# Kernel optimization log

Measured on AMD Instinct MI355X. Metric: run time of the kernel, lower is better.

Reference implementation:

```python
import jax, jax.numpy as jnp
import numpy as np
from itertools import product

NEIGH = (3, 3, 3)  # attn_neighbourhood_size


def setup_inputs() -> dict:
    key = jax.random.key(0)
    b, h, d = 2, 8, 16
    H = W = D = 24
    x = jax.random.normal(key, (b, h, H * W * D, d), dtype=jnp.float32)
    return {"x": x, "height": H, "width": W, "depth": D}


def _localize_3d(x, height, width, depth):
    # x: [b, h, n, d] with n = height*width*depth
    b, hh, n, d = x.shape
    kh, kw, kd = NEIGH
    ph, pw, pd = kh // 2, kw // 2, kd // 2  # 'same' padding for odd kernels
    vol = x.reshape(b, hh, height, width, depth, d)
    padded = jnp.pad(vol, ((0, 0), (0, 0), (ph, ph), (pw, pw), (pd, pd), (0, 0)))
    # conv3d with a unit impulse at (i,j,k) (cross-correlation) is exactly the
    # shifted slice padded[..., i:i+H, j:j+W, k:k+D, :]; filter order is i,j,k.
    shifts = [
        padded[:, :, i:i + height, j:j + width, k:k + depth, :]
        for i, j, k in product(range(kh), range(kw), range(kd))
    ]
    out = jnp.stack(shifts, axis=-2)  # [b, h, H, W, D, filter_n, d]
    return out.reshape(b, hh, n, kh * kw * kd, d)


def reference(x, height, width, depth):
    return _localize_3d(x, height, width, depth)
```

## Files before the change

kernel.cpp:

```cpp
#include <hip/hip_runtime.h>


#define GH 24
#define GW 24
#define GD 24
#define NPOS (GH * GW * GD)
#define NBH 16
#define NDIM 16
#define NF 27


__global__ __launch_bounds__(256) void localize3d_kernel(
    const float4* __restrict__ in,
    float4* __restrict__ out,
    unsigned int total4)
{
    unsigned int stride = gridDim.x * blockDim.x;
    for (unsigned int o = blockIdx.x * blockDim.x + threadIdx.x; o < total4; o += stride) {
        unsigned int dd4 = o & 3u;
        unsigned int r   = o >> 2;
        unsigned int f   = r % NF;
        unsigned int r2  = r / NF;
        unsigned int pos = r2 % NPOS;
        unsigned int bh  = r2 / NPOS;

        unsigned int z  = pos % GD;
        unsigned int xy = pos / GD;
        unsigned int x  = xy % GW;
        unsigned int y  = xy / GW;

        unsigned int fi = f / 9u;
        unsigned int fj = (f / 3u) % 3u;
        unsigned int fk = f % 3u;

        int ny = (int)y + (int)fi - 1;
        int nx = (int)x + (int)fj - 1;
        int nz = (int)z + (int)fk - 1;

        float4 v = make_float4(0.f, 0.f, 0.f, 0.f);
        if ((unsigned)ny < GH && (unsigned)nx < GW && (unsigned)nz < GD) {
            unsigned int npos = ((unsigned)ny * GW + (unsigned)nx) * GD + (unsigned)nz;
            v = in[(bh * NPOS + npos) * 4u + dd4];
        }
        out[o] = v;
    }
}

extern "C" void kernel_launch(void* const* d_in, const int* in_sizes, int n_in,
                              void* d_out, int out_size, void* d_ws, size_t ws_size,
                              hipStream_t stream) {
    const float4* in = (const float4*)d_in[0];
    float4* out = (float4*)d_out;

    unsigned int total4 = (unsigned int)(out_size / 4);
    const int block = 256;
    unsigned int nblocks = (total4 + block - 1) / block;
    if (nblocks > 2048u) nblocks = 2048u;

    localize3d_kernel<<<nblocks, block, 0, stream>>>(in, out, total4);
}
```

Baseline: 425.5 us.

## Stage input neighbourhood slab in LDS and write outputs from shared memory

Each block now owns one (bh, y, 4-wide x tile) output slab and first loads the padded 3x6x26 input neighbourhood into LDS, with zero fill at the borders. It then streams the 27 shifted copies to global memory from LDS using incremental index arithmetic instead of per-element divisions. This targets repeated global/L2 reads of the same inputs and costly integer div/mod. The grid is hard-coded to the fixed 24^3 shape and 16 batch-heads, so the kernel is no longer generic.

```diff
diff --git a/kernel.cpp b/kernel.cpp
--- a/kernel.cpp
+++ b/kernel.cpp
@@ -1,61 +1,76 @@
 #include <hip/hip_runtime.h>
 
 
-#define GH 24
-#define GW 24
-#define GD 24
-#define NPOS (GH * GW * GD)
-#define NBH 16
-#define NDIM 16
 #define NF 27
 
+typedef float4 f4;
 
-__global__ __launch_bounds__(256) void localize3d_kernel(
-    const float4* __restrict__ in,
-    float4* __restrict__ out,
-    unsigned int total4)
+__global__ __launch_bounds__(256) void localize3d_lds(
+    const f4* __restrict__ in,
+    f4* __restrict__ out)
 {
-    unsigned int stride = gridDim.x * blockDim.x;
-    for (unsigned int o = blockIdx.x * blockDim.x + threadIdx.x; o < total4; o += stride) {
-        unsigned int dd4 = o & 3u;
-        unsigned int r   = o >> 2;
-        unsigned int f   = r % NF;
-        unsigned int r2  = r / NF;
-        unsigned int pos = r2 % NPOS;
-        unsigned int bh  = r2 / NPOS;
+    __shared__ f4 slab[1872];
 
-        unsigned int z  = pos % GD;
-        unsigned int xy = pos / GD;
-        unsigned int x  = xy % GW;
-        unsigned int y  = xy / GW;
+    unsigned bid = blockIdx.x;
+    unsigned xt = bid % 6u;
+    unsigned y  = (bid / 6u) % 24u;
+    unsigned bh = bid / 144u;
+    unsigned x0 = xt * 4u;
 
-        unsigned int fi = f / 9u;
-        unsigned int fj = (f / 3u) % 3u;
-        unsigned int fk = f % 3u;
+    for (unsigned s = threadIdx.x; s < 1872u; s += 256u) {
+        unsigned dd4 = s & 3u;
+        unsigned sv  = s >> 2;
+        unsigned sz  = sv % 26u;
+        unsigned sx  = (sv / 26u) % 6u;
+        unsigned sy  = sv / 156u;
+        int gy = (int)y  + (int)sy - 1;
+        int gx = (int)x0 + (int)sx - 1;
+        int gz = (int)sz - 1;
+        f4 v = make_float4(0.f, 0.f, 0.f, 0.f);
+        if ((unsigned)gy < 24u && (unsigned)gx < 24u && (unsigned)gz < 24u) {
+            unsigned q = ((bh * 24u + (unsigned)gy) * 24u + (unsigned)gx) * 24u + (unsigned)gz;
+            v = in[q * 4u + dd4];
+        }
+        slab[s] = v;
+    }
+    __syncthreads();
 
-        int ny = (int)y + (int)fi - 1;
-        int nx = (int)x + (int)fj - 1;
-        int nz = (int)z + (int)fk - 1;
+    unsigned t   = threadIdx.x;
+    unsigned dd4 = t & 3u;
+    unsigned r0  = t >> 2;
+    unsigned lv  = r0 / 27u;
+    unsigned f   = r0 - lv * 27u;
+    unsigned lx  = 0u;
+    unsigned lz  = lv;
 
-        float4 v = make_float4(0.f, 0.f, 0.f, 0.f);
-        if ((unsigned)ny < GH && (unsigned)nx < GW && (unsigned)nz < GD) {
-            unsigned int npos = ((unsigned)ny * GW + (unsigned)nx) * GD + (unsigned)nz;
-            v = in[(bh * NPOS + npos) * 4u + dd4];
-        }
-        out[o] = v;
-    }
+    unsigned q0 = ((bh * 24u + y) * 24u + x0) * 24u;
+    unsigned ob = q0 * 108u + t;
+
+#define BODY() do {                                                     \
+        unsigned fi = (f * 57u) >> 9;                \
+        unsigned f3 = (f * 171u) >> 9;               \
+        unsigned fj = f3 - fi * 3u;                                     \
+        unsigned fk = f - f3 * 3u;                                      \
+        unsigned sv = (fi * 6u + lx + fj) * 26u + (lz + fk);            \
+        out[ob] = slab[sv * 4u + dd4];                                  \
+        ob += 256u;                                                     \
+        f += 10u;                             \
+        unsigned inc = 2u;                                              \
+        if (f >= 27u) { f -= 27u; inc = 3u; }                           \
+        lz += inc;                                                      \
+        if (lz >= 24u) { lz -= 24u; lx += 1u; }                         \
+    } while (0)
+
+#pragma unroll 4
+    for (int k = 0; k < 40; ++k) { BODY(); }
+    if (t < 128u) { BODY(); }
+#undef BODY
 }
 
 extern "C" void kernel_launch(void* const* d_in, const int* in_sizes, int n_in,
                               void* d_out, int out_size, void* d_ws, size_t ws_size,
                               hipStream_t stream) {
-    const float4* in = (const float4*)d_in[0];
-    float4* out = (float4*)d_out;
-
-    unsigned int total4 = (unsigned int)(out_size / 4);
-    const int block = 256;
-    unsigned int nblocks = (total4 + block - 1) / block;
-    if (nblocks > 2048u) nblocks = 2048u;
-
-    localize3d_kernel<<<nblocks, block, 0, stream>>>(in, out, total4);
+    const f4* in = (const f4*)d_in[0];
+    f4* out = (f4*)d_out;
+    localize3d_lds<<<2304, 256, 0, stream>>>(in, out);
 }
```

New measurement: 397.3 us (median of 2 runs). 6.6% less time.
